# Kernel optimization log

Hardware: AMD Instinct MI355X
Metric: run time of the kernel (lower is better)

Reference implementation:

```python
import jax, jax.numpy as jnp
from jax import lax
import numpy as np

N = 256              # total neurons
EPG_LO, EPG_HI = 0, 64      # epg population slice
PEN_LO, PEN_HI = 64, 128    # pen population slice (two hemispheres of 32)
HEMI = 32                    # hemisphere_length_penalty = len(pen)/2
T = 512              # Euler integration steps
B = 1024             # batch of independent trajectories
DT = 0.01            # integration step (seconds)
TAU0 = 0.02          # default time constant (seconds)


def setup_inputs() -> dict:
    key = jax.random.key(0)
    k_w, k_v, k_l = jax.random.split(key, 3)
    W = jax.random.normal(k_w, (N, N), dtype=jnp.float32) * 0.1
    log_scale = jnp.zeros((), dtype=jnp.float32)          # exp(0)=1, initial_weight_scale=1.0
    gain = jnp.ones((N,), dtype=jnp.float32)              # per-neuron gain mask (exp of per-pop params)
    bias = jnp.zeros((N,), dtype=jnp.float32)
    log_tau = jnp.full((N,), np.log(TAU0), dtype=jnp.float32)  # exp -> tau = 0.02
    velocity_scaling = jnp.float32(0.1)
    landmark_scaling = jnp.float32(0.1)
    velocity = jax.random.normal(k_v, (T, B, 2), dtype=jnp.float32)
    landmarks = jax.random.uniform(k_l, (T, B, EPG_HI - EPG_LO), dtype=jnp.float32)
    return {"W": W, "log_scale": log_scale, "gain": gain, "bias": bias,
            "log_tau": log_tau, "velocity_scaling": velocity_scaling,
            "landmark_scaling": landmark_scaling, "velocity": velocity,
            "landmarks": landmarks}


def reference(W, log_scale, gain, bias, log_tau, velocity_scaling,
              landmark_scaling, velocity, landmarks):
    # Effective recurrent weights: sum over blocks of exp(scale)*masked block
    # collapses to exp(log_scale) * W when all block scalings are tied.
    W_eff = jnp.exp(log_scale) * W                      # [N, N]
    tau = jnp.exp(log_tau)                              # [N]
    coef = DT / tau                                     # [N] Euler dt/tau

    def step(state, xs):                                # state: [B, N]
        v, lm = xs                                      # v: [B, 2], lm: [B, 64]
        ext = jnp.zeros((B, N), dtype=state.dtype)
        # landmark input -> epg neurons
        ext = ext.at[:, EPG_LO:EPG_HI].set(lm * landmark_scaling)
        # angular velocity -> pen neurons, split by hemisphere
        ext = ext.at[:, PEN_LO:PEN_LO + HEMI].set(v[:, :1] * velocity_scaling)
        ext = ext.at[:, PEN_LO + HEMI:PEN_HI].set(v[:, 1:2] * velocity_scaling)
        total = state @ W_eff + ext                     # [B, N]
        rate = jax.nn.relu(gain * total + bias)
        new_state = state + coef * (rate - state)       # leaky Euler update
        return new_state, None

    state0 = jnp.zeros((B, N), dtype=jnp.float32)
    final, _ = lax.scan(step, state0, (velocity, landmarks))
    return final[:, EPG_LO:EPG_HI]                      # epg output, [B, 64]
```

## Files before the change

kernel.cpp:

```cpp
#include <hip/hip_runtime.h>

#define NN 256
#define TT 512
#define BB 1024
#define DTC 0.01f

typedef _Float16 half8 __attribute__((ext_vector_type(8)));
typedef float f32x4 __attribute__((ext_vector_type(4)));

__device__ __forceinline__ f32x4 mfma_z(half8 a, half8 b) {
  f32x4 d;
  asm("v_mfma_f32_16x16x32_f16 %0, %1, %2, 0" : "=v"(d) : "a"(a), "v"(b));
  return d;
}
__device__ __forceinline__ void mfma_p(f32x4& c, half8 a, half8 b) {
  asm("v_mfma_f32_16x16x32_f16 %0, %1, %2, %0" : "+v"(c) : "a"(a), "v"(b));
}

template <int CTRL>
__device__ __forceinline__ float rormax(float x) {
  int yi = __builtin_amdgcn_update_dpp(0, __float_as_int(x), CTRL, 0xf, 0xf, false);
  return fmaxf(x, __int_as_float(yi));
}

__global__ __launch_bounds__(256, 1) void ring_attractor_kernel(
    const float* __restrict__ W, const float* __restrict__ log_scale,
    const float* __restrict__ gain, const float* __restrict__ bias,
    const float* __restrict__ log_tau, const float* __restrict__ vscale_p,
    const float* __restrict__ lscale_p, const float* __restrict__ velocity,
    const float* __restrict__ landmarks, float* __restrict__ out) {
  __shared__ __align__(16) _Float16 fragH[2][4096];
  __shared__ __align__(16) _Float16 fragL[2][4096];
  __shared__ __align__(16) float maxslot[2][4];

  const int tid = threadIdx.x;
  const int w  = tid >> 6;
  const int l  = tid & 63;
  const int g  = l >> 4;
  const int li = l & 15;
  const int br = blockIdx.x * 16 + li;

  const float es  = expf(log_scale[0]);
  const float vs  = vscale_p[0];
  const float lms = lscale_p[0];

  float gain_r[4][4], bias_r[4][4], coef_r[4][4];
#pragma unroll
  for (int nt = 0; nt < 4; ++nt)
#pragma unroll
    for (int q = 0; q < 4; ++q) {
      int c = w * 64 + nt * 16 + g * 4 + q;
      gain_r[nt][q] = gain[c];
      bias_r[nt][q] = bias[c];
      coef_r[nt][q] = DTC / expf(log_tau[c]);
    }

  half8 whi[4][8], wlo[4][8];
#pragma unroll
  for (int nt = 0; nt < 4; ++nt)
#pragma unroll
    for (int ks = 0; ks < 8; ++ks) {
      half8 hi, lo;
#pragma unroll
      for (int j = 0; j < 8; ++j) {
        int k = ks * 32 + g * 4 + (j & 3) + ((j >> 2) << 4);
        int m = w * 64 + nt * 16 + li;
        float wv = W[k * NN + m] * es;
        _Float16 h = (_Float16)wv;
        hi[j] = h;
        lo[j] = (_Float16)(wv - (float)h);
      }
      whi[nt][ks] = hi;
      wlo[nt][ks] = lo;
    }

  float s_r[4][4];
#pragma unroll
  for (int nt = 0; nt < 4; ++nt)
#pragma unroll
    for (int q = 0; q < 4; ++q) s_r[nt][q] = 0.f;

  const int wb0 = ((w * 2 + 0) * 64 + g * 16 + li) * 8;
  const int wb1 = ((w * 2 + 1) * 64 + g * 16 + li) * 8;
  {
    half8 z;
#pragma unroll
    for (int j = 0; j < 8; ++j) z[j] = (_Float16)0.f;
    *reinterpret_cast<half8*>(&fragH[0][wb0]) = z;
    *reinterpret_cast<half8*>(&fragH[0][wb1]) = z;
    *reinterpret_cast<half8*>(&fragL[0][wb0]) = z;
    *reinterpret_cast<half8*>(&fragL[0][wb1]) = z;
    if (tid < 8) maxslot[tid >> 2][tid & 3] = 0.f;
  }
  float inv_scale = 1.f;
  float amPrev = 0.f;

  f32x4 eA0{}, eA1{}, eA2{}, eA3{}, eB0{}, eB1{}, eB2{}, eB3{};
  if (w == 0) {
    const float* p = landmarks + (size_t)br * 64 + g * 4;
    eA0 = *reinterpret_cast<const f32x4*>(p);
    eA1 = *reinterpret_cast<const f32x4*>(p + 16);
    eA2 = *reinterpret_cast<const f32x4*>(p + 32);
    eA3 = *reinterpret_cast<const f32x4*>(p + 48);
  } else if (w == 1) {
    const float* p = velocity + (size_t)br * 2;
    eA0[0] = p[0];
    eA0[1] = p[1];
  }
  __syncthreads();

#define STEP(T, CUR, E0, E1, E2, E3, P0, P1, P2, P3)                           \
  {                                                                            \
      \
    {                                                                          \
      float r = amPrev;                                                        \
      r = rormax<0x121>(r);                                                    \
      r = rormax<0x122>(r);                                                    \
      r = rormax<0x124>(r);                                                    \
      r = rormax<0x128>(r);                                                    \
      r = fmaxf(r, __shfl_xor(r, 16));                                         \
      r = fmaxf(r, __shfl_xor(r, 32));                                         \
      if (l == 0) maxslot[CUR][w] = r;                                         \
    }                                                                          \
                        \
    float M;                                                                   \
    {                                                                          \
      f32x4 mv = *reinterpret_cast<const f32x4*>(&maxslot[CUR ^ 1][0]);        \
      M = fmaxf(fmaxf(mv[0], mv[1]), fmaxf(mv[2], mv[3]));                     \
    }                                                                          \
                                     \
    {                                                                          \
      const int tn = (T) + 1 < TT ? (T) + 1 : TT - 1;                          \
      if (w == 0) {                                                            \
        const float* p = landmarks + ((size_t)tn * BB + br) * 64 + g * 4;      \
        P0 = *reinterpret_cast<const f32x4*>(p);                               \
        P1 = *reinterpret_cast<const f32x4*>(p + 16);                          \
        P2 = *reinterpret_cast<const f32x4*>(p + 32);                          \
        P3 = *reinterpret_cast<const f32x4*>(p + 48);                          \
      } else if (w == 1) {                                                     \
        const float* p = velocity + ((size_t)tn * BB + br) * 2;                \
        P0[0] = p[0];                                                          \
        P0[1] = p[1];                                                          \
      }                                                                        \
    }                                                                          \
                 \
    f32x4 a0h, a1h, a2h, a3h, a0l, a1l, a2l, a3l, a0c, a1c, a2c, a3c;          \
    _Pragma("unroll")                                                          \
    for (int ks = 0; ks < 8; ++ks) {                                           \
      const int rb = (ks * 64 + g * 16 + li) * 8;                              \
      half8 bh = *reinterpret_cast<const half8*>(&fragH[CUR][rb]);             \
      half8 bl = *reinterpret_cast<const half8*>(&fragL[CUR][rb]);             \
      if (ks == 0) {                                                           \
        a0h = mfma_z(whi[0][0], bh);                                           \
        a1h = mfma_z(whi[1][0], bh);                                           \
        a2h = mfma_z(whi[2][0], bh);                                           \
        a3h = mfma_z(whi[3][0], bh);                                           \
        a0l = mfma_z(wlo[0][0], bh);                                           \
        a1l = mfma_z(wlo[1][0], bh);                                           \
        a2l = mfma_z(wlo[2][0], bh);                                           \
        a3l = mfma_z(wlo[3][0], bh);                                           \
        a0c = mfma_z(whi[0][0], bl);                                           \
        a1c = mfma_z(whi[1][0], bl);                                           \
        a2c = mfma_z(whi[2][0], bl);                                           \
        a3c = mfma_z(whi[3][0], bl);                                           \
      } else {                                                                 \
        mfma_p(a0h, whi[0][ks], bh);                                           \
        mfma_p(a1h, whi[1][ks], bh);                                           \
        mfma_p(a2h, whi[2][ks], bh);                                           \
        mfma_p(a3h, whi[3][ks], bh);                                           \
        mfma_p(a0l, wlo[0][ks], bh);                                           \
        mfma_p(a1l, wlo[1][ks], bh);                                           \
        mfma_p(a2l, wlo[2][ks], bh);                                           \
        mfma_p(a3l, wlo[3][ks], bh);                                           \
        mfma_p(a0c, whi[0][ks], bl);                                           \
        mfma_p(a1c, whi[1][ks], bl);                                           \
        mfma_p(a2c, whi[2][ks], bl);                                           \
        mfma_p(a3c, whi[3][ks], bl);                                           \
      }                                                                        \
    }                                                                          \
    asm volatile("s_nop 7\n\ts_nop 7"                                          \
                 : "+v"(a0h), "+v"(a1h), "+v"(a2h), "+v"(a3h), "+v"(a0l),      \
                   "+v"(a1l), "+v"(a2l), "+v"(a3l), "+v"(a0c), "+v"(a1c),      \
                   "+v"(a2c), "+v"(a3c));                                      \
          \
    float scale_n, inv_n;                                                      \
    {                                                                          \
      int e = 134 - (int)(__float_as_uint(M) >> 23);                           \
      e = e > 9 ? 9 : e;                                                       \
      scale_n = __int_as_float((e + 127) << 23);                               \
      inv_n = __int_as_float((127 - e) << 23);                                 \
    }                                                                          \
                                    \
    float am = 0.f;                                                            \
    _Pragma("unroll")                                                          \
    for (int nt = 0; nt < 4; ++nt) {                                           \
      f32x4 av = (nt == 0) ? (a0h + a0l + a0c)                                 \
               : (nt == 1) ? (a1h + a1l + a1c)                                 \
               : (nt == 2) ? (a2h + a2l + a2c)                                 \
                           : (a3h + a3l + a3c);                                \
      _Pragma("unroll")                                                        \
      for (int q = 0; q < 4; ++q) {                                            \
        float ext;                                                             \
        if (w == 0) {                                                          \
          f32x4 ev = (nt == 0) ? E0 : (nt == 1) ? E1 : (nt == 2) ? E2 : E3;    \
          ext = lms * ev[q];                                                   \
        } else if (w == 1) {                                                   \
          ext = vs * ((nt < 2) ? E0[0] : E0[1]);                               \
        } else {                                                               \
          ext = 0.f;                                                           \
        }                                                                      \
        float tot = __builtin_fmaf(av[q], inv_scale, ext);                     \
        float rate = fmaxf(__builtin_fmaf(gain_r[nt][q], tot, bias_r[nt][q]),  \
                           0.f);                                               \
        float sv = s_r[nt][q];                                                 \
        sv = __builtin_fmaf(coef_r[nt][q], rate - sv, sv);                     \
        s_r[nt][q] = sv;                                                       \
        am = fmaxf(am, fabsf(sv));                                             \
      }                                                                        \
    }                                                                          \
    amPrev = am;                                                               \
             \
    half8 h0, h1, l0, l1;                                                      \
    _Pragma("unroll")                                                          \
    for (int j = 0; j < 8; ++j) {                                              \
      float sc0 = s_r[j >> 2][j & 3] * scale_n;                                \
      float sc1 = s_r[2 + (j >> 2)][j & 3] * scale_n;                          \
      _Float16 q0 = (_Float16)sc0;                                             \
      _Float16 q1 = (_Float16)sc1;                                             \
      h0[j] = q0;                                                              \
      l0[j] = (_Float16)(sc0 - (float)q0);                                     \
      h1[j] = q1;                                                              \
      l1[j] = (_Float16)(sc1 - (float)q1);                                     \
    }                                                                          \
    *reinterpret_cast<half8*>(&fragH[CUR ^ 1][wb0]) = h0;                      \
    *reinterpret_cast<half8*>(&fragH[CUR ^ 1][wb1]) = h1;                      \
    *reinterpret_cast<half8*>(&fragL[CUR ^ 1][wb0]) = l0;                      \
    *reinterpret_cast<half8*>(&fragL[CUR ^ 1][wb1]) = l1;                      \
    inv_scale = inv_n;                                                         \
    __syncthreads();                                                           \
  }

#pragma unroll 1
  for (int t = 0; t < TT; t += 2) {
    STEP(t, 0, eA0, eA1, eA2, eA3, eB0, eB1, eB2, eB3)
    STEP(t + 1, 1, eB0, eB1, eB2, eB3, eA0, eA1, eA2, eA3)
  }
#undef STEP

  if (w == 0) {
#pragma unroll
    for (int nt = 0; nt < 4; ++nt) {
      f32x4 o;
#pragma unroll
      for (int q = 0; q < 4; ++q) o[q] = s_r[nt][q];
      *reinterpret_cast<f32x4*>(out + (size_t)br * 64 + nt * 16 + g * 4) = o;
    }
  }
}

extern "C" void kernel_launch(void* const* d_in, const int* in_sizes, int n_in,
                              void* d_out, int out_size, void* d_ws, size_t ws_size,
                              hipStream_t stream) {
  const float* W         = (const float*)d_in[0];
  const float* log_scale = (const float*)d_in[1];
  const float* gain      = (const float*)d_in[2];
  const float* bias      = (const float*)d_in[3];
  const float* log_tau   = (const float*)d_in[4];
  const float* vscale    = (const float*)d_in[5];
  const float* lscale    = (const float*)d_in[6];
  const float* velocity  = (const float*)d_in[7];
  const float* landmarks = (const float*)d_in[8];
  float* out = (float*)d_out;

  ring_attractor_kernel<<<dim3(BB / 16), dim3(256), 0, stream>>>(
      W, log_scale, gain, bias, log_tau, vscale, lscale, velocity, landmarks, out);
}
```

Measured before the change: 691.9 us.

## Interleave final-k MFMAs with per-tile epilogue and early fragment stores

Loads all eight B fragments from LDS up front, then splits the last k-step of MFMAs per output tile so the elementwise Euler update for tile 0/1 overlaps the remaining MFMAs for tiles 2/3. The fp16 hi/lo fragment writes for the first half are issued as soon as their state is ready, and the scale computation is hoisted before the matmul. The goal is to hide MFMA latency and the long s_nop drain on the serial per-step critical path, at the cost of more live registers for the preloaded fragments.

```diff
diff --git a/kernel.cpp b/kernel.cpp
--- a/kernel.cpp
+++ b/kernel.cpp
@@ -109,6 +109,30 @@
   }
   __syncthreads();
 
+#define TAIL(NT, AH, AL, AC, E0, E1, E2, E3)                                   \
+  {                                                                            \
+    f32x4 av = (AH + AL) + AC;                                                 \
+    _Pragma("unroll")                                                          \
+    for (int q = 0; q < 4; ++q) {                                              \
+      float ext;                                                               \
+      if (w == 0) {                                                            \
+        f32x4 ev = (NT == 0) ? E0 : (NT == 1) ? E1 : (NT == 2) ? E2 : E3;      \
+        ext = lms * ev[q];                                                     \
+      } else if (w == 1) {                                                     \
+        ext = vs * ((NT < 2) ? E0[0] : E0[1]);                                 \
+      } else {                                                                 \
+        ext = 0.f;                                                             \
+      }                                                                        \
+      float tot = __builtin_fmaf(av[q], inv_scale, ext);                       \
+      float rate = fmaxf(__builtin_fmaf(gain_r[NT][q], tot, bias_r[NT][q]),    \
+                         0.f);                                                 \
+      float sv = s_r[NT][q];                                                   \
+      sv = __builtin_fmaf(coef_r[NT][q], rate - sv, sv);                       \
+      s_r[NT][q] = sv;                                                         \
+      am = fmaxf(am, fabsf(sv));                                               \
+    }                                                                          \
+  }
+
 #define STEP(T, CUR, E0, E1, E2, E3, P0, P1, P2, P3)                           \
   {                                                                            \
       \
@@ -122,11 +146,15 @@
       r = fmaxf(r, __shfl_xor(r, 32));                                         \
       if (l == 0) maxslot[CUR][w] = r;                                         \
     }                                                                          \
-                        \
-    float M;                                                                   \
+           \
+    float scale_n, inv_n;                                                      \
     {                                                                          \
       f32x4 mv = *reinterpret_cast<const f32x4*>(&maxslot[CUR ^ 1][0]);        \
-      M = fmaxf(fmaxf(mv[0], mv[1]), fmaxf(mv[2], mv[3]));                     \
+      float M = fmaxf(fmaxf(mv[0], mv[1]), fmaxf(mv[2], mv[3]));               \
+      int e = 134 - (int)(__float_as_uint(M) >> 23);                           \
+      e = e > 9 ? 9 : e;                                                       \
+      scale_n = __int_as_float((e + 127) << 23);                               \
+      inv_n = __int_as_float((127 - e) << 23);                                 \
     }                                                                          \
                                      \
     {                                                                          \
@@ -143,99 +171,90 @@
         P0[1] = p[1];                                                          \
       }                                                                        \
     }                                                                          \
-                 \
-    f32x4 a0h, a1h, a2h, a3h, a0l, a1l, a2l, a3l, a0c, a1c, a2c, a3c;          \
+         \
+    half8 bhr[8], blr[8];                                                      \
     _Pragma("unroll")                                                          \
     for (int ks = 0; ks < 8; ++ks) {                                           \
       const int rb = (ks * 64 + g * 16 + li) * 8;                              \
-      half8 bh = *reinterpret_cast<const half8*>(&fragH[CUR][rb]);             \
-      half8 bl = *reinterpret_cast<const half8*>(&fragL[CUR][rb]);             \
-      if (ks == 0) {                                                           \
-        a0h = mfma_z(whi[0][0], bh);                                           \
-        a1h = mfma_z(whi[1][0], bh);                                           \
-        a2h = mfma_z(whi[2][0], bh);                                           \
-        a3h = mfma_z(whi[3][0], bh);                                           \
-        a0l = mfma_z(wlo[0][0], bh);                                           \
-        a1l = mfma_z(wlo[1][0], bh);                                           \
-        a2l = mfma_z(wlo[2][0], bh);                                           \
-        a3l = mfma_z(wlo[3][0], bh);                                           \
-        a0c = mfma_z(whi[0][0], bl);                                           \
-        a1c = mfma_z(whi[1][0], bl);                                           \
-        a2c = mfma_z(whi[2][0], bl);                                           \
-        a3c = mfma_z(whi[3][0], bl);                                           \
-      } else {                                                                 \
-        mfma_p(a0h, whi[0][ks], bh);                                           \
-        mfma_p(a1h, whi[1][ks], bh);                                           \
-        mfma_p(a2h, whi[2][ks], bh);                                           \
-        mfma_p(a3h, whi[3][ks], bh);                                           \
-        mfma_p(a0l, wlo[0][ks], bh);                                           \
-        mfma_p(a1l, wlo[1][ks], bh);                                           \
-        mfma_p(a2l, wlo[2][ks], bh);                                           \
-        mfma_p(a3l, wlo[3][ks], bh);                                           \
-        mfma_p(a0c, whi[0][ks], bl);                                           \
-        mfma_p(a1c, whi[1][ks], bl);                                           \
-        mfma_p(a2c, whi[2][ks], bl);                                           \
-        mfma_p(a3c, whi[3][ks], bl);                                           \
-      }                                                                        \
-    }                                                                          \
-    asm volatile("s_nop 7\n\ts_nop 7"                                          \
-                 : "+v"(a0h), "+v"(a1h), "+v"(a2h), "+v"(a3h), "+v"(a0l),      \
-                   "+v"(a1l), "+v"(a2l), "+v"(a3l), "+v"(a0c), "+v"(a1c),      \
-                   "+v"(a2c), "+v"(a3c));                                      \
-          \
-    float scale_n, inv_n;                                                      \
-    {                                                                          \
-      int e = 134 - (int)(__float_as_uint(M) >> 23);                           \
-      e = e > 9 ? 9 : e;                                                       \
-      scale_n = __int_as_float((e + 127) << 23);                               \
-      inv_n = __int_as_float((127 - e) << 23);                                 \
-    }                                                                          \
-                                    \
+      bhr[ks] = *reinterpret_cast<const half8*>(&fragH[CUR][rb]);              \
+      blr[ks] = *reinterpret_cast<const half8*>(&fragL[CUR][rb]);              \
+    }                                                                          \
+                   \
+    f32x4 a0h, a1h, a2h, a3h, a0l, a1l, a2l, a3l, a0c, a1c, a2c, a3c;          \
+    a0h = mfma_z(whi[0][0], bhr[0]);                                           \
+    a1h = mfma_z(whi[1][0], bhr[0]);                                           \
+    a2h = mfma_z(whi[2][0], bhr[0]);                                           \
+    a3h = mfma_z(whi[3][0], bhr[0]);                                           \
+    a0l = mfma_z(wlo[0][0], bhr[0]);                                           \
+    a1l = mfma_z(wlo[1][0], bhr[0]);                                           \
+    a2l = mfma_z(wlo[2][0], bhr[0]);                                           \
+    a3l = mfma_z(wlo[3][0], bhr[0]);                                           \
+    a0c = mfma_z(whi[0][0], blr[0]);                                           \
+    a1c = mfma_z(whi[1][0], blr[0]);                                           \
+    a2c = mfma_z(whi[2][0], blr[0]);                                           \
+    a3c = mfma_z(whi[3][0], blr[0]);                                           \
+    _Pragma("unroll")                                                          \
+    for (int ks = 1; ks < 7; ++ks) {                                           \
+      mfma_p(a0h, whi[0][ks], bhr[ks]);                                        \
+      mfma_p(a1h, whi[1][ks], bhr[ks]);                                        \
+      mfma_p(a2h, whi[2][ks], bhr[ks]);                                        \
+      mfma_p(a3h, whi[3][ks], bhr[ks]);                                        \
+      mfma_p(a0l, wlo[0][ks], bhr[ks]);                                        \
+      mfma_p(a1l, wlo[1][ks], bhr[ks]);                                        \
+      mfma_p(a2l, wlo[2][ks], bhr[ks]);                                        \
+      mfma_p(a3l, wlo[3][ks], bhr[ks]);                                        \
+      mfma_p(a0c, whi[0][ks], blr[ks]);                                        \
+      mfma_p(a1c, whi[1][ks], blr[ks]);                                        \
+      mfma_p(a2c, whi[2][ks], blr[ks]);                                        \
+      mfma_p(a3c, whi[3][ks], blr[ks]);                                        \
+    }                                                                          \
+               \
     float am = 0.f;                                                            \
-    _Pragma("unroll")                                                          \
-    for (int nt = 0; nt < 4; ++nt) {                                           \
-      f32x4 av = (nt == 0) ? (a0h + a0l + a0c)                                 \
-               : (nt == 1) ? (a1h + a1l + a1c)                                 \
-               : (nt == 2) ? (a2h + a2l + a2c)                                 \
-                           : (a3h + a3l + a3c);                                \
+    mfma_p(a0h, whi[0][7], bhr[7]);                                            \
+    mfma_p(a0l, wlo[0][7], bhr[7]);                                            \
+    mfma_p(a0c, whi[0][7], blr[7]);                                            \
+    mfma_p(a1h, whi[1][7], bhr[7]);                                            \
+    mfma_p(a1l, wlo[1][7], bhr[7]);                                            \
+    mfma_p(a1c, whi[1][7], blr[7]);                                            \
+    asm volatile("s_nop 7" : "+v"(a0h), "+v"(a0l), "+v"(a0c));                 \
+    TAIL(0, a0h, a0l, a0c, E0, E1, E2, E3)                                     \
+    mfma_p(a2h, whi[2][7], bhr[7]);                                            \
+    mfma_p(a2l, wlo[2][7], bhr[7]);                                            \
+    mfma_p(a2c, whi[2][7], blr[7]);                                            \
+    TAIL(1, a1h, a1l, a1c, E0, E1, E2, E3)                                     \
+    mfma_p(a3h, whi[3][7], bhr[7]);                                            \
+    mfma_p(a3l, wlo[3][7], bhr[7]);                                            \
+    mfma_p(a3c, whi[3][7], blr[7]);                                            \
+            \
+    {                                                                          \
+      half8 h0, l0;                                                            \
       _Pragma("unroll")                                                        \
-      for (int q = 0; q < 4; ++q) {                                            \
-        float ext;                                                             \
-        if (w == 0) {                                                          \
-          f32x4 ev = (nt == 0) ? E0 : (nt == 1) ? E1 : (nt == 2) ? E2 : E3;    \
-          ext = lms * ev[q];                                                   \
-        } else if (w == 1) {                                                   \
-          ext = vs * ((nt < 2) ? E0[0] : E0[1]);                               \
-        } else {                                                               \
-          ext = 0.f;                                                           \
-        }                                                                      \
-        float tot = __builtin_fmaf(av[q], inv_scale, ext);                     \
-        float rate = fmaxf(__builtin_fmaf(gain_r[nt][q], tot, bias_r[nt][q]),  \
-                           0.f);                                               \
-        float sv = s_r[nt][q];                                                 \
-        sv = __builtin_fmaf(coef_r[nt][q], rate - sv, sv);                     \
-        s_r[nt][q] = sv;                                                       \
-        am = fmaxf(am, fabsf(sv));                                             \
-      }                                                                        \
+      for (int j = 0; j < 8; ++j) {                                            \
+        float sc0 = s_r[j >> 2][j & 3] * scale_n;                              \
+        _Float16 q0 = (_Float16)sc0;                                           \
+        h0[j] = q0;                                                            \
+        l0[j] = (_Float16)(sc0 - (float)q0);                                   \
+      }                                                                        \
+      *reinterpret_cast<half8*>(&fragH[CUR ^ 1][wb0]) = h0;                    \
+      *reinterpret_cast<half8*>(&fragL[CUR ^ 1][wb0]) = l0;                    \
+    }                                                                          \
+    TAIL(2, a2h, a2l, a2c, E0, E1, E2, E3)                                     \
+    asm volatile("s_nop 7" : "+v"(a3h), "+v"(a3l), "+v"(a3c));                 \
+    TAIL(3, a3h, a3l, a3c, E0, E1, E2, E3)                                     \
+                                      \
+    {                                                                          \
+      half8 h1, l1;                                                            \
+      _Pragma("unroll")                                                        \
+      for (int j = 0; j < 8; ++j) {                                            \
+        float sc1 = s_r[2 + (j >> 2)][j & 3] * scale_n;                        \
+        _Float16 q1 = (_Float16)sc1;                                           \
+        h1[j] = q1;                                                            \
+        l1[j] = (_Float16)(sc1 - (float)q1);                                   \
+      }                                                                        \
+      *reinterpret_cast<half8*>(&fragH[CUR ^ 1][wb1]) = h1;                    \
+      *reinterpret_cast<half8*>(&fragL[CUR ^ 1][wb1]) = l1;                    \
     }                                                                          \
     amPrev = am;                                                               \
-             \
-    half8 h0, h1, l0, l1;                                                      \
-    _Pragma("unroll")                                                          \
-    for (int j = 0; j < 8; ++j) {                                              \
-      float sc0 = s_r[j >> 2][j & 3] * scale_n;                                \
-      float sc1 = s_r[2 + (j >> 2)][j & 3] * scale_n;                          \
-      _Float16 q0 = (_Float16)sc0;                                             \
-      _Float16 q1 = (_Float16)sc1;                                             \
-      h0[j] = q0;                                                              \
-      l0[j] = (_Float16)(sc0 - (float)q0);                                     \
-      h1[j] = q1;                                                              \
-      l1[j] = (_Float16)(sc1 - (float)q1);                                     \
-    }                                                                          \
-    *reinterpret_cast<half8*>(&fragH[CUR ^ 1][wb0]) = h0;                      \
-    *reinterpret_cast<half8*>(&fragH[CUR ^ 1][wb1]) = h1;                      \
-    *reinterpret_cast<half8*>(&fragL[CUR ^ 1][wb0]) = l0;                      \
-    *reinterpret_cast<half8*>(&fragL[CUR ^ 1][wb1]) = l1;                      \
     inv_scale = inv_n;                                                         \
     __syncthreads();                                                           \
   }
@@ -246,6 +265,7 @@
     STEP(t + 1, 1, eB0, eB1, eB2, eB3, eA0, eA1, eA2, eA3)
   }
 #undef STEP
+#undef TAIL
 
   if (w == 0) {
 #pragma unroll
```

New measurement: 684.3 us. No clear change (-1.1%).
